# Kernel optimization log

Hardware: AMD Instinct MI355X
Metric: run time of the kernel (lower is better)

The kernel has to match this reference:

```python
import jax, jax.numpy as jnp
import numpy as np

N, E, G, IN, H, L, C = 20000, 320000, 128, 16, 64, 4, 10
AVG_D_LOG = float(np.log(17.0))  # log(avg_degree + 1)


def setup_inputs() -> dict:
    key = jax.random.key(0)
    ks = jax.random.split(key, 24)
    p = lambda k, shape: jax.random.normal(k, shape, dtype=jnp.float32) * 0.05
    return dict(
        h=jax.random.normal(ks[0], (N, IN), jnp.float32),
        snorm_n=jax.random.uniform(ks[1], (N, 1), jnp.float32, 0.05, 1.0),
        embW=p(ks[2], (IN, H)), embB=p(ks[3], (H,)),
        preW=p(ks[4], (L, 2 * H, H)), preB=p(ks[5], (L, H)),
        postW=p(ks[6], (L, 13 * H, H)), postB=p(ks[7], (L, H)),
        mixW=p(ks[8], (L, H, H)), mixB=p(ks[9], (L, H)),
        r1W=p(ks[10], (H, H // 2)), r1B=p(ks[11], (H // 2,)),
        r2W=p(ks[12], (H // 2, H // 4)), r2B=p(ks[13], (H // 4,)),
        r3W=p(ks[14], (H // 4, C)), r3B=p(ks[15], (C,)),
        src=jax.random.randint(ks[16], (E,), 0, N),
        dst=jax.random.randint(ks[17], (E,), 0, N),
        graph_ids=jnp.sort(jax.random.randint(ks[18], (N,), 0, G)),
    )


def _pna_forward(h, snorm_n, embW, embB, preW, preB, postW, postB, mixW, mixB,
                 r1W, r1B, r2W, r2B, r3W, r3B, src, dst, graph_ids):
    # Degree-based scalers (computed once; graph is fixed across layers)
    deg = jax.ops.segment_sum(jnp.ones((E,), h.dtype), dst, num_segments=N)  # [N]
    degc = jnp.maximum(deg, 1.0)[:, None]
    logd = jnp.log(deg + 1.0)
    amp = (logd / AVG_D_LOG)[:, None]                      # amplification scaler
    att = (AVG_D_LOG / jnp.maximum(logd, 1e-5))[:, None]   # attenuation scaler
    has_nb = (deg > 0.0)[:, None]

    x = h @ embW + embB  # node embedding [N, H]
    for i in range(L):
        x_in = x
        # pretrans: per-edge message from cat(h_src, h_dst)  [E, H]
        m = jnp.concatenate([x[src], x[dst]], axis=-1) @ preW[i] + preB[i]
        # multi-aggregator reduce at dst: mean, max, min, std
        mean = jax.ops.segment_sum(m, dst, num_segments=N) / degc
        msq = jax.ops.segment_sum(m * m, dst, num_segments=N) / degc
        std = jnp.sqrt(jax.nn.relu(msq - mean * mean) + 1e-5)
        mx = jnp.where(has_nb, jax.ops.segment_max(m, dst, num_segments=N), 0.0)
        mn = jnp.where(has_nb, jax.ops.segment_min(m, dst, num_segments=N), 0.0)
        agg = jnp.concatenate([mean, mx, mn, std], axis=-1)  # [N, 4H]
        # degree scalers: identity, amplification, attenuation -> [N, 12H]
        scaled = jnp.concatenate([agg, agg * amp, agg * att], axis=-1)
        # posttrans over cat(scaled_agg, h) -> [N, H]
        y = jnp.concatenate([scaled, x], axis=-1) @ postW[i] + postB[i]
        # tower mixing network (LeakyReLU FC)
        y = jax.nn.leaky_relu(y @ mixW[i] + mixB[i])
        y = y * snorm_n          # graph norm
        x = x_in + y             # residual
    # mean-nodes readout per graph
    gsum = jax.ops.segment_sum(x, graph_ids, num_segments=G)
    cnt = jnp.maximum(jax.ops.segment_sum(jnp.ones((N,), x.dtype), graph_ids, num_segments=G), 1.0)
    hg = gsum / cnt[:, None]
    # MLPReadout: two halving ReLU layers + classifier
    hg = jax.nn.relu(hg @ r1W + r1B)
    hg = jax.nn.relu(hg @ r2W + r2B)
    return hg @ r3W + r3B  # [G, C]


def reference(h, snorm_n, embW, embB, preW, preB, postW, postB, mixW, mixB,
              r1W, r1B, r2W, r2B, r3W, r3B, src, dst, graph_ids):
    return _pna_forward(h, snorm_n, embW, embB, preW, preB, postW, postB,
                        mixW, mixB, r1W, r1B, r2W, r2B, r3W, r3B,
                        src, dst, graph_ids)
```

## Files before the change

### kernel.cpp

```cpp
#include <hip/hip_runtime.h>
#include <math.h>

#define N_ 20000
#define E_ 320000
#define G_ 128
#define IN_ 16
#define H_ 64
#define L_ 4
#define C_ 10
#define AVG_D_LOG 2.8332133440562162f

union F4 { float4 v; float f[4]; };

typedef _Float16 h8 __attribute__((ext_vector_type(8)));
typedef _Float16 h4 __attribute__((ext_vector_type(4)));
typedef float f4x __attribute__((ext_vector_type(4)));
#define MFMA16(a, b, c) __builtin_amdgcn_mfma_f32_16x16x32_f16((a), (b), (c), 0, 0, 0)


__global__ __launch_bounds__(256) void k_setup(
    const float* __restrict__ h, const float* __restrict__ embW, const float* __restrict__ embB,
    float* __restrict__ x,
    const float* __restrict__ preW, const float* __restrict__ postW, const float* __restrict__ mixW,
    _Float16* __restrict__ preWT, _Float16* __restrict__ postWT, _Float16* __restrict__ mixWT,
    int* __restrict__ zbase) {
  int bb = blockIdx.x, tid = threadIdx.x;
  if (bb < 5000) {
    int n = bb * 4 + (tid >> 6);
    int c = tid & 63;
    float acc = embB[c];
#pragma unroll
    for (int k = 0; k < IN_; k++) acc += h[n * IN_ + k] * embW[k * H_ + c];
    x[n * H_ + c] = acc;
  } else if (bb < 6024) {
    int idx = (bb - 5000) * 256 + tid;
    if (idx < 32768) {
      int l = idx >> 13, r = idx & 8191;
      int c = r >> 6, k = r & 63;
      preWT[idx] = (_Float16)preW[l * 8192 + k * 64 + c];
    } else if (idx < 245760) {
      int j = idx - 32768;
      int l = j / 53248, r = j % 53248;
      int c = r / 832, k = r % 832;
      postWT[j] = (_Float16)postW[l * 53248 + k * 64 + c];
    } else {
      int j = idx - 245760;
      int l = j >> 12, r = j & 4095;
      int c = r >> 6, k = r & 63;
      mixWT[j] = (_Float16)mixW[l * 4096 + k * 64 + c];
    }
  } else {
    int i = (bb - 6024) * 256 + tid;
    if (i < 2 * N_) zbase[i] = 0;
  }
}


__global__ __launch_bounds__(256) void k_hist(const int* __restrict__ dst, int* __restrict__ deg) {
  int e = blockIdx.x * 256 + threadIdx.x;
  if (e < E_) atomicAdd(&deg[dst[e]], 1);
}


__global__ __launch_bounds__(1024) void k_scan(const int* __restrict__ deg, int* __restrict__ offs) {
  __shared__ int sh[1024];
  int t = threadIdx.x;
  int base = t * 20;
  int local[20];
  int s = 0;
#pragma unroll
  for (int i = 0; i < 20; i++) {
    int idx = base + i;
    int v = (idx < N_) ? deg[idx] : 0;
    local[i] = s; s += v;
  }
  sh[t] = s;
  __syncthreads();
  for (int off = 1; off < 1024; off <<= 1) {
    int v = (t >= off) ? sh[t - off] : 0;
    __syncthreads();
    sh[t] += v;
    __syncthreads();
  }
  int excl = sh[t] - s;
#pragma unroll
  for (int i = 0; i < 20; i++) {
    int idx = base + i;
    if (idx < N_) offs[idx] = excl + local[i];
  }
  if (t == 0) offs[N_] = sh[1023];
}


__global__ __launch_bounds__(256) void k_mix(
    const int* __restrict__ src, const int* __restrict__ dst,
    const int* __restrict__ offs, int* __restrict__ cursor, int* __restrict__ csr,
    const int* __restrict__ deg,
    float* __restrict__ ampv, float* __restrict__ attv,
    float* __restrict__ invd, float* __restrict__ hnb,
    const float* __restrict__ x, const _Float16* __restrict__ preWT,
    const float* __restrict__ preB, _Float16* __restrict__ ah, float* __restrict__ b) {
  int bb = blockIdx.x, tid = threadIdx.x;
  if (bb < 1250) {
    int e = bb * 256 + tid;
    if (e < E_) {
      int d = dst[e];
      int pos = offs[d] + atomicAdd(&cursor[d], 1);
      csr[pos] = src[e];
    }
  } else if (bb < 1329) {
    int idx = (bb - 1250) * 256 + tid;
    if (idx < N_) {
      float d = (float)deg[idx];
      float logd = logf(d + 1.f);
      ampv[idx] = logd / AVG_D_LOG;
      attv[idx] = AVG_D_LOG / fmaxf(logd, 1e-5f);
      invd[idx] = 1.f / fmaxf(d, 1.f);
      hnb[idx] = d > 0.f ? 1.f : 0.f;
    }
  } else {
    int n0 = (bb - 1329) * 32;
    int lane = tid & 63, wv = tid >> 6;
    int mt = wv & 1, nh = wv >> 1;
    int l15 = lane & 15, k0q = (lane >> 4) * 8;
    int mrow = n0 + mt * 16 + l15;
    const float* xr = x + (size_t)mrow * 64;
    const _Float16* wb0 = preWT + (size_t)(nh * 64 + l15) * 64 + k0q;
    f4x acc0 = {0.f,0.f,0.f,0.f}, acc1 = {0.f,0.f,0.f,0.f}, acc2 = {0.f,0.f,0.f,0.f}, acc3 = {0.f,0.f,0.f,0.f};
#pragma unroll
    for (int kb = 0; kb < 64; kb += 32) {
      int ko = kb + k0q;
      F4 xa, xb2;
      xa.v = *(const float4*)(xr + ko);
      xb2.v = *(const float4*)(xr + ko + 4);
      h8 af;
      af[0]=(_Float16)xa.f[0]; af[1]=(_Float16)xa.f[1]; af[2]=(_Float16)xa.f[2]; af[3]=(_Float16)xa.f[3];
      af[4]=(_Float16)xb2.f[0]; af[5]=(_Float16)xb2.f[1]; af[6]=(_Float16)xb2.f[2]; af[7]=(_Float16)xb2.f[3];
      acc0 = MFMA16(af, *(const h8*)(wb0 + kb), acc0);
      acc1 = MFMA16(af, *(const h8*)(wb0 + 1024 + kb), acc1);
      acc2 = MFMA16(af, *(const h8*)(wb0 + 2048 + kb), acc2);
      acc3 = MFMA16(af, *(const h8*)(wb0 + 3072 + kb), acc3);
    }
    int rbase = n0 + mt * 16 + (lane >> 4) * 4;
    f4x accs[4] = {acc0, acc1, acc2, acc3};
#pragma unroll
    for (int t = 0; t < 4; t++) {
      int col = nh * 64 + t * 16 + l15;
#pragma unroll
      for (int r = 0; r < 4; r++) {
        int n = rbase + r;
        if (col < 64) ah[(size_t)n * 64 + col] = (_Float16)accs[t][r];
        else          b[(size_t)n * 64 + (col - 64)] = accs[t][r] + preB[col - 64];
      }
    }
  }
}


__global__ __launch_bounds__(256) void k_layer(
    const _Float16* __restrict__ ahin, const float* __restrict__ bin,
    const int* __restrict__ offs, const int* __restrict__ csr,
    const float* __restrict__ invd, const float* __restrict__ hnb,
    const _Float16* __restrict__ WT, const float* __restrict__ Bv,
    const _Float16* __restrict__ mixWT, const float* __restrict__ mixB,
    const float* __restrict__ ampv, const float* __restrict__ attv,
    const float* __restrict__ snorm, float* __restrict__ x,
    const _Float16* __restrict__ preWT, const float* __restrict__ preB,
    _Float16* __restrict__ ahout, float* __restrict__ bout, int do_pre) {
  __shared__ _Float16 aggs[16 * 272];
  __shared__ _Float16 ys[16 * 80];
  __shared__ _Float16 xs[16 * 80];
  int tid = threadIdx.x;
  int n0 = blockIdx.x * 16;
  int lane = tid & 63, wv = tid >> 6;

  {
    int nl = tid >> 4, q = tid & 15;
    int n = n0 + nl;
    int o0 = offs[n];
    int deg = offs[n + 1] - o0;
    float sum[4], sq[4], mx[4], mn[4];
#pragma unroll
    for (int i = 0; i < 4; i++) {
      sum[i] = 0.f; sq[i] = 0.f;
      mx[i] = -__builtin_inff(); mn[i] = __builtin_inff();
    }
    int j = 0;
    for (; j + 3 < deg; j += 4) {
      int s0 = csr[o0 + j];
      int s1 = csr[o0 + j + 1];
      int s2 = csr[o0 + j + 2];
      int s3 = csr[o0 + j + 3];
      h4 a0 = *(const h4*)(ahin + (size_t)s0 * 64 + q * 4);
      h4 a1 = *(const h4*)(ahin + (size_t)s1 * 64 + q * 4);
      h4 a2 = *(const h4*)(ahin + (size_t)s2 * 64 + q * 4);
      h4 a3 = *(const h4*)(ahin + (size_t)s3 * 64 + q * 4);
#pragma unroll
      for (int i = 0; i < 4; i++) {
        float v0 = (float)a0[i], v1 = (float)a1[i], v2 = (float)a2[i], v3 = (float)a3[i];
        sum[i] += (v0 + v1) + (v2 + v3);
        sq[i] += v0 * v0;
        sq[i] += v1 * v1;
        sq[i] += v2 * v2;
        sq[i] += v3 * v3;
        mx[i] = fmaxf(mx[i], fmaxf(fmaxf(v0, v1), fmaxf(v2, v3)));
        mn[i] = fminf(mn[i], fminf(fminf(v0, v1), fminf(v2, v3)));
      }
    }
    for (; j < deg; j++) {
      int s0 = csr[o0 + j];
      h4 a0 = *(const h4*)(ahin + (size_t)s0 * 64 + q * 4);
#pragma unroll
      for (int i = 0; i < 4; i++) {
        float v0 = (float)a0[i];
        sum[i] += v0;
        sq[i] += v0 * v0;
        mx[i] = fmaxf(mx[i], v0);
        mn[i] = fminf(mn[i], v0);
      }
    }
    float inv = invd[n], hn = hnb[n];
    F4 bv; bv.v = *(const float4*)(bin + (size_t)n * 64 + q * 4);
    h4 hm, hx, hmn, hs;
#pragma unroll
    for (int i = 0; i < 4; i++) {
      float mean_a = sum[i] * inv;
      float var = sq[i] * inv - mean_a * mean_a;
      hs[i] = (_Float16)sqrtf(fmaxf(var, 0.f) + 1e-5f);
      bool nb = hn > 0.5f;
      hm[i] = (_Float16)(nb ? (mean_a + bv.f[i]) : 0.f);
      hx[i] = (_Float16)(nb ? (mx[i] + bv.f[i]) : 0.f);
      hmn[i] = (_Float16)(nb ? (mn[i] + bv.f[i]) : 0.f);
    }
    _Float16* ap = aggs + nl * 272 + q * 4;
    *(h4*)(ap) = hm;
    *(h4*)(ap + 64) = hx;
    *(h4*)(ap + 128) = hmn;
    *(h4*)(ap + 192) = hs;
  }
  __syncthreads();

  int nh = wv;
  int l15 = lane & 15, k0q = (lane >> 4) * 8;
  int mrow = n0 + l15;
  const _Float16* ag = aggs + (size_t)l15 * 272 + k0q;
  int col0 = nh * 16 + l15;
  const _Float16* w0 = WT + (size_t)col0 * 832 + k0q;
  f4x aI = {0.f,0.f,0.f,0.f}, aA = {0.f,0.f,0.f,0.f}, aT = {0.f,0.f,0.f,0.f};
#pragma unroll 4
  for (int kb = 0; kb < 256; kb += 32) {
    h8 af = *(const h8*)(ag + kb);
    aI = MFMA16(af, *(const h8*)(w0 + kb), aI);
    aA = MFMA16(af, *(const h8*)(w0 + 256 + kb), aA);
    aT = MFMA16(af, *(const h8*)(w0 + 512 + kb), aT);
  }
  const float* xr = x + (size_t)mrow * 64;
#pragma unroll
  for (int kb = 0; kb < 64; kb += 32) {
    int ko = kb + k0q;
    F4 xa, xb2;
    xa.v = *(const float4*)(xr + ko);
    xb2.v = *(const float4*)(xr + ko + 4);
    h8 af;
    af[0]=(_Float16)xa.f[0]; af[1]=(_Float16)xa.f[1]; af[2]=(_Float16)xa.f[2]; af[3]=(_Float16)xa.f[3];
    af[4]=(_Float16)xb2.f[0]; af[5]=(_Float16)xb2.f[1]; af[6]=(_Float16)xb2.f[2]; af[7]=(_Float16)xb2.f[3];
    aI = MFMA16(af, *(const h8*)(w0 + 768 + kb), aI);
  }
  int qr = (lane >> 4) * 4;
  int rbase = n0 + qr;
  int yrow = qr;
  float b0 = Bv[col0];
#pragma unroll
  for (int r = 0; r < 4; r++) {
    int n = rbase + r;
    float amp = ampv[n], att = attv[n];
    ys[(yrow + r) * 80 + col0] = (_Float16)(aI[r] + b0 + amp * aA[r] + att * aT[r]);
  }
  __syncthreads();
  f4x m0 = {0.f,0.f,0.f,0.f};
  const _Float16* yr = ys + (size_t)l15 * 80 + k0q;
  const _Float16* mw0 = mixWT + (size_t)col0 * 64 + k0q;
#pragma unroll
  for (int kb = 0; kb < 64; kb += 32) {
    h8 af = *(const h8*)(yr + kb);
    m0 = MFMA16(af, *(const h8*)(mw0 + kb), m0);
  }
  float mb0 = mixB[col0];
#pragma unroll
  for (int r = 0; r < 4; r++) {
    int n = rbase + r;
    float sn = snorm[n];
    float t0 = m0[r] + mb0; t0 = t0 > 0.f ? t0 : 0.01f * t0;
    float* xp = x + (size_t)n * 64;
    float xo0 = xp[col0] + t0 * sn;
    xp[col0] = xo0;
    xs[(yrow + r) * 80 + col0] = (_Float16)xo0;
  }

  if (do_pre) {
    __syncthreads();
    int ch = wv;
    const _Float16* xf = xs + (size_t)l15 * 80 + k0q;
    const _Float16* wb0 = preWT + (size_t)(ch * 32 + l15) * 64 + k0q;
    f4x p0 = {0.f,0.f,0.f,0.f}, p1 = {0.f,0.f,0.f,0.f};
#pragma unroll
    for (int kb = 0; kb < 64; kb += 32) {
      h8 af = *(const h8*)(xf + kb);
      p0 = MFMA16(af, *(const h8*)(wb0 + kb), p0);
      p1 = MFMA16(af, *(const h8*)(wb0 + 1024 + kb), p1);
    }
    int prb = n0 + (lane >> 4) * 4;
    f4x accs[2] = {p0, p1};
#pragma unroll
    for (int t = 0; t < 2; t++) {
      int col = ch * 32 + t * 16 + l15;
#pragma unroll
      for (int r = 0; r < 4; r++) {
        int n = prb + r;
        if (col < 64) ahout[(size_t)n * 64 + col] = (_Float16)accs[t][r];
        else          bout[(size_t)n * 64 + (col - 64)] = accs[t][r] + preB[col - 64];
      }
    }
  }
}


__device__ inline int lower_bound_gid(const int* __restrict__ gid, int val) {
  int lo = 0, hi = N_;
  while (lo < hi) {
    int mid = (lo + hi) >> 1;
    if (gid[mid] < val) lo = mid + 1; else hi = mid;
  }
  return lo;
}

__global__ __launch_bounds__(256) void k_readout_fused(
    const float* __restrict__ x, const int* __restrict__ gid,
    const float* __restrict__ r1W, const float* __restrict__ r1B,
    const float* __restrict__ r2W, const float* __restrict__ r2B,
    const float* __restrict__ r3W, const float* __restrict__ r3B,
    float* __restrict__ out) {
  __shared__ float part[4 * 64];
  __shared__ float hg[64];
  __shared__ float t1[32];
  __shared__ float t2[16];
  int g = blockIdx.x, tid = threadIdx.x;
  int lo = lower_bound_gid(gid, g);
  int hi = lower_bound_gid(gid, g + 1);
  int c = tid & 63, w = tid >> 6;
  float s = 0.f;
  for (int n = lo + w; n < hi; n += 4) s += x[(size_t)n * 64 + c];
  part[w * 64 + c] = s;
  __syncthreads();
  if (w == 0) {
    float tot = part[c] + part[64 + c] + part[128 + c] + part[192 + c];
    float cnt = (float)(hi - lo);
    if (cnt < 1.f) cnt = 1.f;
    hg[c] = tot / cnt;
  }
  __syncthreads();
  if (tid < 32) {
    float acc = r1B[tid];
#pragma unroll 8
    for (int k = 0; k < 64; k++) acc += hg[k] * r1W[k * 32 + tid];
    t1[tid] = fmaxf(acc, 0.f);
  }
  __syncthreads();
  if (tid < 16) {
    float acc = r2B[tid];
#pragma unroll 8
    for (int k = 0; k < 32; k++) acc += t1[k] * r2W[k * 16 + tid];
    t2[tid] = fmaxf(acc, 0.f);
  }
  __syncthreads();
  if (tid < 10) {
    float acc = r3B[tid];
#pragma unroll
    for (int k = 0; k < 16; k++) acc += t2[k] * r3W[k * 10 + tid];
    out[g * 10 + tid] = acc;
  }
}


extern "C" void kernel_launch(void* const* d_in, const int* in_sizes, int n_in,
                              void* d_out, int out_size, void* d_ws, size_t ws_size,
                              hipStream_t stream) {
  const float* h     = (const float*)d_in[0];
  const float* snorm = (const float*)d_in[1];
  const float* embW  = (const float*)d_in[2];
  const float* embB  = (const float*)d_in[3];
  const float* preW  = (const float*)d_in[4];
  const float* preB  = (const float*)d_in[5];
  const float* postW = (const float*)d_in[6];
  const float* postB = (const float*)d_in[7];
  const float* mixW  = (const float*)d_in[8];
  const float* mixB  = (const float*)d_in[9];
  const float* r1W   = (const float*)d_in[10];
  const float* r1B   = (const float*)d_in[11];
  const float* r2W   = (const float*)d_in[12];
  const float* r2B   = (const float*)d_in[13];
  const float* r3W   = (const float*)d_in[14];
  const float* r3B   = (const float*)d_in[15];
  const int* src     = (const int*)d_in[16];
  const int* dst     = (const int*)d_in[17];
  const int* gid     = (const int*)d_in[18];
  float* out = (float*)d_out;

  char* w = (char*)d_ws;
  float* x        = (float*)w; w += (size_t)N_ * 64 * 4;
  _Float16* ah0   = (_Float16*)w; w += (size_t)N_ * 64 * 2;
  _Float16* ah1   = (_Float16*)w; w += (size_t)N_ * 64 * 2;
  float* b0       = (float*)w; w += (size_t)N_ * 64 * 4;
  float* b1       = (float*)w; w += (size_t)N_ * 64 * 4;
  _Float16* preWT = (_Float16*)w; w += (size_t)4 * 128 * 64 * 2;
  _Float16* postWT= (_Float16*)w; w += (size_t)4 * 64 * 832 * 2;
  _Float16* mixWT = (_Float16*)w; w += (size_t)4 * 64 * 64 * 2;
  float* ampv = (float*)w; w += (size_t)N_ * 4;
  float* attv = (float*)w; w += (size_t)N_ * 4;
  float* invd = (float*)w; w += (size_t)N_ * 4;
  float* hnb  = (float*)w; w += (size_t)N_ * 4;
  int* csr    = (int*)w;   w += (size_t)E_ * 4;
  int* offs   = (int*)w;   w += (size_t)(N_ + 64) * 4;
  int* zbase  = (int*)w;
  int* deg    = (int*)w;   w += (size_t)N_ * 4;
  int* cursor = (int*)w;   w += (size_t)N_ * 4;

  k_setup<<<6181, 256, 0, stream>>>(h, embW, embB, x, preW, postW, mixW,
                                    preWT, postWT, mixWT, zbase);
  k_hist<<<E_ / 256, 256, 0, stream>>>(dst, deg);
  k_scan<<<1, 1024, 0, stream>>>(deg, offs);
  k_mix<<<1250 + 79 + 625, 256, 0, stream>>>(src, dst, offs, cursor, csr, deg,
                                             ampv, attv, invd, hnb,
                                             x, preWT, preB, ah0, b0);
  int gb = N_ / 16;
  _Float16* ahs[2] = {ah0, ah1};
  float* bs[2] = {b0, b1};
  for (int l = 0; l < L_; l++) {
    int pin = l & 1, pout = 1 - pin;
    k_layer<<<gb, 256, 0, stream>>>(ahs[pin], bs[pin], offs, csr, invd, hnb,
                                    postWT + (size_t)l * 53248, postB + l * H_,
                                    mixWT + (size_t)l * 4096, mixB + l * H_,
                                    ampv, attv, snorm, x,
                                    preWT + (size_t)(l + 1 < L_ ? l + 1 : 0) * 8192,
                                    preB + (l + 1 < L_ ? l + 1 : 0) * H_,
                                    ahs[pout], bs[pout], l + 1 < L_ ? 1 : 0);
  }
  k_readout_fused<<<G_, 256, 0, stream>>>(x, gid, r1W, r1B, r2W, r2B, r3W, r3B, out);
}
```

Before: 303.2 us.

## Shrink layer blocks to 8 nodes with 128 threads, two column tiles per wave

The per-layer kernel now handles 8 nodes per block with 2 waves instead of 16 nodes with 4 waves. Each wave computes two 16-column output tiles for the posttrans, mix and pretrans MFMAs. Because the 16-row MFMA tiles are only half filled, rows past 8 are masked off at the stores. The goal is more blocks and finer-grained scheduling of the irregular gather phase, but it doubles weight-load traffic per node and wastes half of the MFMA work on padding rows.

Result: slower. 395.0 us (+30.3%).

```diff
diff --git a/kernel.cpp b/kernel.cpp
--- a/kernel.cpp
+++ b/kernel.cpp
@@ -157,7 +157,7 @@
 }
 
 
-__global__ __launch_bounds__(256) void k_layer(
+__global__ __launch_bounds__(128) void k_layer(
     const _Float16* __restrict__ ahin, const float* __restrict__ bin,
     const int* __restrict__ offs, const int* __restrict__ csr,
     const float* __restrict__ invd, const float* __restrict__ hnb,
@@ -171,7 +171,7 @@
   __shared__ _Float16 ys[16 * 80];
   __shared__ _Float16 xs[16 * 80];
   int tid = threadIdx.x;
-  int n0 = blockIdx.x * 16;
+  int n0 = blockIdx.x * 8;
   int lane = tid & 63, wv = tid >> 6;
 
   {
@@ -240,19 +240,24 @@
   }
   __syncthreads();
 
-  int nh = wv;
   int l15 = lane & 15, k0q = (lane >> 4) * 8;
-  int mrow = n0 + l15;
+  int mrow = n0 + l15; if (mrow > N_ - 1) mrow = N_ - 1;
   const _Float16* ag = aggs + (size_t)l15 * 272 + k0q;
-  int col0 = nh * 16 + l15;
+  int col0 = wv * 32 + l15;
+  int col1 = col0 + 16;
   const _Float16* w0 = WT + (size_t)col0 * 832 + k0q;
-  f4x aI = {0.f,0.f,0.f,0.f}, aA = {0.f,0.f,0.f,0.f}, aT = {0.f,0.f,0.f,0.f};
+  const _Float16* w1 = WT + (size_t)col1 * 832 + k0q;
+  f4x aI0={0.f,0.f,0.f,0.f}, aA0={0.f,0.f,0.f,0.f}, aT0={0.f,0.f,0.f,0.f};
+  f4x aI1={0.f,0.f,0.f,0.f}, aA1={0.f,0.f,0.f,0.f}, aT1={0.f,0.f,0.f,0.f};
 #pragma unroll 4
   for (int kb = 0; kb < 256; kb += 32) {
     h8 af = *(const h8*)(ag + kb);
-    aI = MFMA16(af, *(const h8*)(w0 + kb), aI);
-    aA = MFMA16(af, *(const h8*)(w0 + 256 + kb), aA);
-    aT = MFMA16(af, *(const h8*)(w0 + 512 + kb), aT);
+    aI0 = MFMA16(af, *(const h8*)(w0 + kb), aI0);
+    aI1 = MFMA16(af, *(const h8*)(w1 + kb), aI1);
+    aA0 = MFMA16(af, *(const h8*)(w0 + 256 + kb), aA0);
+    aA1 = MFMA16(af, *(const h8*)(w1 + 256 + kb), aA1);
+    aT0 = MFMA16(af, *(const h8*)(w0 + 512 + kb), aT0);
+    aT1 = MFMA16(af, *(const h8*)(w1 + 512 + kb), aT1);
   }
   const float* xr = x + (size_t)mrow * 64;
 #pragma unroll
@@ -264,61 +269,73 @@
     h8 af;
     af[0]=(_Float16)xa.f[0]; af[1]=(_Float16)xa.f[1]; af[2]=(_Float16)xa.f[2]; af[3]=(_Float16)xa.f[3];
     af[4]=(_Float16)xb2.f[0]; af[5]=(_Float16)xb2.f[1]; af[6]=(_Float16)xb2.f[2]; af[7]=(_Float16)xb2.f[3];
-    aI = MFMA16(af, *(const h8*)(w0 + 768 + kb), aI);
+    aI0 = MFMA16(af, *(const h8*)(w0 + 768 + kb), aI0);
+    aI1 = MFMA16(af, *(const h8*)(w1 + 768 + kb), aI1);
   }
   int qr = (lane >> 4) * 4;
-  int rbase = n0 + qr;
-  int yrow = qr;
-  float b0 = Bv[col0];
-#pragma unroll
-  for (int r = 0; r < 4; r++) {
-    int n = rbase + r;
-    float amp = ampv[n], att = attv[n];
-    ys[(yrow + r) * 80 + col0] = (_Float16)(aI[r] + b0 + amp * aA[r] + att * aT[r]);
-  }
-  __syncthreads();
-  f4x m0 = {0.f,0.f,0.f,0.f};
+  if (qr < 8) {
+    float b0 = Bv[col0], b1 = Bv[col1];
+#pragma unroll
+    for (int r = 0; r < 4; r++) {
+      int n = n0 + qr + r;
+      float amp = ampv[n], att = attv[n];
+      ys[(qr + r) * 80 + col0] = (_Float16)(aI0[r] + b0 + amp * aA0[r] + att * aT0[r]);
+      ys[(qr + r) * 80 + col1] = (_Float16)(aI1[r] + b1 + amp * aA1[r] + att * aT1[r]);
+    }
+  }
+  __syncthreads();
+  f4x m0 = {0.f,0.f,0.f,0.f}, m1 = {0.f,0.f,0.f,0.f};
   const _Float16* yr = ys + (size_t)l15 * 80 + k0q;
   const _Float16* mw0 = mixWT + (size_t)col0 * 64 + k0q;
+  const _Float16* mw1 = mixWT + (size_t)col1 * 64 + k0q;
 #pragma unroll
   for (int kb = 0; kb < 64; kb += 32) {
     h8 af = *(const h8*)(yr + kb);
     m0 = MFMA16(af, *(const h8*)(mw0 + kb), m0);
-  }
-  float mb0 = mixB[col0];
-#pragma unroll
-  for (int r = 0; r < 4; r++) {
-    int n = rbase + r;
-    float sn = snorm[n];
-    float t0 = m0[r] + mb0; t0 = t0 > 0.f ? t0 : 0.01f * t0;
-    float* xp = x + (size_t)n * 64;
-    float xo0 = xp[col0] + t0 * sn;
-    xp[col0] = xo0;
-    xs[(yrow + r) * 80 + col0] = (_Float16)xo0;
+    m1 = MFMA16(af, *(const h8*)(mw1 + kb), m1);
+  }
+  if (qr < 8) {
+    float mb0 = mixB[col0], mb1 = mixB[col1];
+#pragma unroll
+    for (int r = 0; r < 4; r++) {
+      int n = n0 + qr + r;
+      float sn = snorm[n];
+      float t0 = m0[r] + mb0; t0 = t0 > 0.f ? t0 : 0.01f * t0;
+      float t1 = m1[r] + mb1; t1 = t1 > 0.f ? t1 : 0.01f * t1;
+      float* xp = x + (size_t)n * 64;
+      float xo0 = xp[col0] + t0 * sn;
+      float xo1 = xp[col1] + t1 * sn;
+      xp[col0] = xo0;
+      xp[col1] = xo1;
+      xs[(qr + r) * 80 + col0] = (_Float16)xo0;
+      xs[(qr + r) * 80 + col1] = (_Float16)xo1;
+    }
   }
 
   if (do_pre) {
     __syncthreads();
-    int ch = wv;
     const _Float16* xf = xs + (size_t)l15 * 80 + k0q;
-    const _Float16* wb0 = preWT + (size_t)(ch * 32 + l15) * 64 + k0q;
-    f4x p0 = {0.f,0.f,0.f,0.f}, p1 = {0.f,0.f,0.f,0.f};
+    const _Float16* wb0 = preWT + (size_t)(wv * 64 + l15) * 64 + k0q;
+    f4x p0 = {0.f,0.f,0.f,0.f}, p1 = {0.f,0.f,0.f,0.f}, p2 = {0.f,0.f,0.f,0.f}, p3 = {0.f,0.f,0.f,0.f};
 #pragma unroll
     for (int kb = 0; kb < 64; kb += 32) {
       h8 af = *(const h8*)(xf + kb);
       p0 = MFMA16(af, *(const h8*)(wb0 + kb), p0);
       p1 = MFMA16(af, *(const h8*)(wb0 + 1024 + kb), p1);
-    }
-    int prb = n0 + (lane >> 4) * 4;
-    f4x accs[2] = {p0, p1};
-#pragma unroll
-    for (int t = 0; t < 2; t++) {
-      int col = ch * 32 + t * 16 + l15;
-#pragma unroll
-      for (int r = 0; r < 4; r++) {
-        int n = prb + r;
-        if (col < 64) ahout[(size_t)n * 64 + col] = (_Float16)accs[t][r];
-        else          bout[(size_t)n * 64 + (col - 64)] = accs[t][r] + preB[col - 64];
+      p2 = MFMA16(af, *(const h8*)(wb0 + 2048 + kb), p2);
+      p3 = MFMA16(af, *(const h8*)(wb0 + 3072 + kb), p3);
+    }
+    if (qr < 8) {
+      f4x accs[4] = {p0, p1, p2, p3};
+#pragma unroll
+      for (int t = 0; t < 4; t++) {
+        int col = wv * 64 + t * 16 + l15;
+#pragma unroll
+        for (int r = 0; r < 4; r++) {
+          int n = n0 + qr + r;
+          if (col < 64) ahout[(size_t)n * 64 + col] = (_Float16)accs[t][r];
+          else          bout[(size_t)n * 64 + (col - 64)] = accs[t][r] + preB[col - 64];
+        }
       }
     }
   }
@@ -432,12 +449,12 @@
   k_mix<<<1250 + 79 + 625, 256, 0, stream>>>(src, dst, offs, cursor, csr, deg,
                                              ampv, attv, invd, hnb,
                                              x, preWT, preB, ah0, b0);
-  int gb = N_ / 16;
+  int gb = N_ / 8;
   _Float16* ahs[2] = {ah0, ah1};
   float* bs[2] = {b0, b1};
   for (int l = 0; l < L_; l++) {
     int pin = l & 1, pout = 1 - pin;
-    k_layer<<<gb, 256, 0, stream>>>(ahs[pin], bs[pin], offs, csr, invd, hnb,
+    k_layer<<<gb, 128, 0, stream>>>(ahs[pin], bs[pin], offs, csr, invd, hnb,
                                     postWT + (size_t)l * 53248, postB + l * H_,
                                     mixWT + (size_t)l * 4096, mixB + l * H_,
                                     ampv, attv, snorm, x,
```
